# Kernel tuning notes

Hardware: AMD Instinct MI355X
Metric: run time of the kernel (lower is better)

Reference implementation:

```python
import jax, jax.numpy as jnp
import numpy as np

V, E, H, B, TE, TD = 32000, 256, 256, 32, 128, 64


def _gru_cell(x, h, Wi, Wh, bi, bh):
    # PyTorch GRU gate order: r, z, n
    gi = x @ Wi.T + bi            # [B, 3H]
    gh = h @ Wh.T + bh            # [B, 3H]
    i_r, i_z, i_n = jnp.split(gi, 3, axis=-1)
    h_r, h_z, h_n = jnp.split(gh, 3, axis=-1)
    r = jax.nn.sigmoid(i_r + h_r)
    z = jax.nn.sigmoid(i_z + h_z)
    n = jnp.tanh(i_n + r * h_n)
    return (1.0 - z) * n + z * h


def _run_gru(x_seq, h0, Wi, Wh, bi, bh, reverse=False):
    # x_seq: [B, T, D] -> outputs [B, T, H]
    xs = jnp.swapaxes(x_seq, 0, 1)  # [T, B, D]
    def step(h, x_t):
        h = _gru_cell(x_t, h, Wi, Wh, bi, bh)
        return h, h
    _, ys = jax.lax.scan(step, h0, xs, reverse=reverse)
    return jnp.swapaxes(ys, 0, 1)


def setup_inputs() -> dict:
    key = jax.random.key(0)
    ks = jax.random.split(key, 22)
    k = 1.0 / np.sqrt(H)
    u = lambda kk, shape, a: jax.random.uniform(kk, shape, jnp.float32, -a, a)
    return {
        'enc_in': jax.random.randint(ks[0], (B, TE), 0, V),
        'dec_in': jax.random.randint(ks[1], (B, TD), 0, V),
        'embed_W': u(ks[2], (V, E), 0.1),
        'Wi_f': u(ks[3], (3 * H, E), k), 'Wh_f': u(ks[4], (3 * H, H), k),
        'bi_f': u(ks[5], (3 * H,), k), 'bh_f': u(ks[6], (3 * H,), k),
        'Wi_b': u(ks[7], (3 * H, E), k), 'Wh_b': u(ks[8], (3 * H, H), k),
        'bi_b': u(ks[9], (3 * H,), k), 'bh_b': u(ks[10], (3 * H,), k),
        'Wi_d': u(ks[11], (3 * H, E + 2 * H), k), 'Wh_d': u(ks[12], (3 * H, H), k),
        'bi_d': u(ks[13], (3 * H,), k), 'bh_d': u(ks[14], (3 * H,), k),
        'W1_w': u(ks[15], (H, 2 * H), 1.0 / np.sqrt(2 * H)), 'W1_b': u(ks[16], (H,), 1.0 / np.sqrt(2 * H)),
        'W2_w': u(ks[17], (2 * H, H), k), 'W2_b': u(ks[18], (2 * H,), k),
        'lin_w': u(ks[19], (V, H), 0.1), 'lin_b': jnp.zeros((V,), jnp.float32),
    }


def reference(enc_in, dec_in, embed_W, Wi_f, Wh_f, bi_f, bh_f, Wi_b, Wh_b, bi_b, bh_b,
              Wi_d, Wh_d, bi_d, bh_d, W1_w, W1_b, W2_w, W2_b, lin_w, lin_b):
    # ---- encoder (bidirectional GRU, 1 layer) ----
    enc_emb = embed_W[enc_in]                                   # [B, TE, E]
    h0 = jnp.zeros((B, H), enc_emb.dtype)
    out_f = _run_gru(enc_emb, h0, Wi_f, Wh_f, bi_f, bh_f)       # [B, TE, H]
    out_b = _run_gru(enc_emb, h0, Wi_b, Wh_b, bi_b, bh_b, reverse=True)
    encoded = jnp.concatenate([out_f, out_b], axis=-1)          # [B, TE, 2H]

    # last valid state per example: encoded[i, sizes[i]-1]
    sizes = (enc_in > 0).sum(axis=1)                            # [B]
    last_states = encoded[jnp.arange(B), sizes - 1]             # [B, 2H]

    # ---- decoder with Luong attention (teacher forcing) ----
    dec_emb = embed_W[dec_in]                                   # [B, TD, E]
    h_init = last_states @ W1_w.T + W1_b                        # [B, H]
    ctx_init = jnp.zeros((B, 2 * H), enc_emb.dtype)

    def dec_step(carry, x_t):
        h, ctx = carry
        inp = jnp.concatenate([ctx, x_t], axis=-1)              # [B, E+2H]
        h = _gru_cell(inp, h, Wi_d, Wh_d, bi_d, bh_d)           # [B, H]
        comp = h @ W2_w.T + W2_b                                # [B, 2H]
        scores = jax.nn.softmax(jnp.einsum('bte,be->bt', encoded, comp), axis=-1)
        ctx = jnp.einsum('bt,bte->be', scores, encoded)          # [B, 2H]
        return (h, ctx), h

    _, outs = jax.lax.scan(dec_step, (h_init, ctx_init), jnp.swapaxes(dec_emb, 0, 1))
    outs = jnp.swapaxes(outs, 0, 1)                             # [B, TD, H]
    logits = outs @ lin_w.T + lin_b                             # [B, TD, V]
    return logits
```

## Files before the change

kernel.cpp:

```cpp
#include <hip/hip_runtime.h>
#include <hip/hip_bf16.h>

#define Vv 32000
#define Ee 256
#define Hh 256
#define Bb 32
#define TEe 128
#define TDd 64

typedef __attribute__((ext_vector_type(4))) float f32x4;
typedef __attribute__((ext_vector_type(8))) short short8;
typedef __attribute__((ext_vector_type(2))) unsigned int uint2v;
typedef __attribute__((ext_vector_type(4))) unsigned int uint4v;

static __device__ __forceinline__ unsigned short f2bf(float f){
  unsigned u = __float_as_uint(f);
  u += 0x7fffu + ((u >> 16) & 1u);
  return (unsigned short)(u >> 16);
}
static __device__ __forceinline__ unsigned pack2(float a, float b){
  return ((unsigned)f2bf(b) << 16) | (unsigned)f2bf(a);
}
static __device__ __forceinline__ float dot8(uint4v u, const float* hh){
  float s = 0.f;
  #pragma unroll
  for (int i = 0; i < 4; ++i){
    unsigned w = u[i];
    s = fmaf(__uint_as_float(w << 16),        hh[2*i],   s);
    s = fmaf(__uint_as_float(w & 0xffff0000u), hh[2*i+1], s);
  }
  return s;
}
static __device__ __forceinline__ float sigmoidf_(float x){
  return 1.f / (1.f + __expf(-x));
}

__global__ void k_sizes(const int* __restrict__ enc_in, int* __restrict__ sizes){
  int b = threadIdx.x;
  if (b < Bb){
    int c = 0;
    for (int t = 0; t < TEe; ++t) c += (enc_in[b*TEe + t] > 0);
    sizes[b] = c;
  }
}

__global__ void k_gather(const int* __restrict__ tok, const float* __restrict__ embW,
                         float* __restrict__ out, int rows){
  int i = blockIdx.x * 256 + threadIdx.x;
  int r = i >> 8, c = i & 255;
  if (r < rows) out[i] = embW[(size_t)tok[r]*Ee + c];
}

__global__ void k_extract_bf16(const float* __restrict__ src, unsigned short* __restrict__ dst,
                               int n){
  int i = blockIdx.x * 256 + threadIdx.x;
  if (i < n) dst[i] = f2bf(src[i]);
}

__global__ void k_chunkw(const float* __restrict__ src, unsigned short* __restrict__ dst, int rows){
  int idx = blockIdx.x * 256 + threadIdx.x;
  if (idx < rows * 256){
    int i = idx & 7, r = (idx >> 3) % rows, kb = idx / (rows * 8);
    dst[idx] = f2bf(src[(size_t)r*256 + kb*8 + i]);
  }
}

__global__ void k_projchunk(const float* __restrict__ in, unsigned short* __restrict__ out){
  int idx = blockIdx.x * 256 + threadIdx.x;
  int i = idx & 7;
  int t1 = idx >> 3;
  int n = t1 % 768;
  int t2 = t1 / 768;
  int kb = t2 & 15, b = t2 >> 4;
  out[idx] = f2bf(in[(size_t)(b*TEe + kb*8 + i)*768 + n]);
}

template<bool A_BF16, bool B_BF16, bool B_KMAJOR, bool OUT_BF16>
__global__ __launch_bounds__(256) void k_gemm(
  const void* __restrict__ Av, const void* __restrict__ Bv,
  const float* __restrict__ bias, void* __restrict__ Cv,
  int M, int N, int K, int lda, int ldb, int ldc)
{
  __shared__ unsigned short lA[128*40];
  __shared__ unsigned short lB[128*40];
  const int tid  = threadIdx.x;
  const int lane = tid & 63;
  const int w = tid >> 6, wr = w >> 1, wc = w & 1;
  const int m0 = blockIdx.y * 128, n0 = blockIdx.x * 128;
  f32x4 acc[4][4];
  #pragma unroll
  for (int i = 0; i < 4; ++i)
    #pragma unroll
    for (int j = 0; j < 4; ++j) acc[i][j] = (f32x4){0.f,0.f,0.f,0.f};

  for (int k0 = 0; k0 < K; k0 += 32){
    if (A_BF16){
      const unsigned short* A = (const unsigned short*)Av;
      #pragma unroll
      for (int it = 0; it < 2; ++it){
        int idx = tid + it*256; int r = idx >> 2, q = idx & 3;
        *(uint4v*)&lA[r*40 + q*8] = *(const uint4v*)(A + (size_t)(m0+r)*lda + k0 + q*8);
      }
    } else {
      const float* A = (const float*)Av;
      #pragma unroll
      for (int it = 0; it < 4; ++it){
        int idx = tid + it*256; int r = idx >> 3, q = idx & 7;
        f32x4 v = *(const f32x4*)(A + (size_t)(m0+r)*lda + k0 + q*4);
        uint2v pk; pk[0] = pack2(v[0], v[1]); pk[1] = pack2(v[2], v[3]);
        *(uint2v*)&lA[r*40 + q*4] = pk;
      }
    }
    if (B_KMAJOR){
      const float* Bp = (const float*)Bv;
      #pragma unroll
      for (int it = 0; it < 4; ++it){
        int idx = tid + it*256; int kk = idx >> 5, nq = idx & 31;
        f32x4 v = *(const f32x4*)(Bp + (size_t)(k0+kk)*ldb + n0 + nq*4);
        #pragma unroll
        for (int s2 = 0; s2 < 4; ++s2) lB[(nq*4+s2)*40 + kk] = f2bf(v[s2]);
      }
    } else if (B_BF16){
      const unsigned short* Bp = (const unsigned short*)Bv;
      #pragma unroll
      for (int it = 0; it < 2; ++it){
        int idx = tid + it*256; int r = idx >> 2, q = idx & 3;
        *(uint4v*)&lB[r*40 + q*8] = *(const uint4v*)(Bp + (size_t)(n0+r)*ldb + k0 + q*8);
      }
    } else {
      const float* Bp = (const float*)Bv;
      #pragma unroll
      for (int it = 0; it < 4; ++it){
        int idx = tid + it*256; int r = idx >> 3, q = idx & 7;
        f32x4 v = *(const f32x4*)(Bp + (size_t)(n0+r)*ldb + k0 + q*4);
        uint2v pk; pk[0] = pack2(v[0], v[1]); pk[1] = pack2(v[2], v[3]);
        *(uint2v*)&lB[r*40 + q*4] = pk;
      }
    }
    __syncthreads();
    short8 av[4], bv[4];
    #pragma unroll
    for (int i = 0; i < 4; ++i)
      av[i] = *(const short8*)&lA[(wr*64 + i*16 + (lane&15))*40 + (lane>>4)*8];
    #pragma unroll
    for (int j = 0; j < 4; ++j)
      bv[j] = *(const short8*)&lB[(wc*64 + j*16 + (lane&15))*40 + (lane>>4)*8];
    #pragma unroll
    for (int i = 0; i < 4; ++i)
      #pragma unroll
      for (int j = 0; j < 4; ++j)
        acc[i][j] = __builtin_amdgcn_mfma_f32_16x16x32_bf16(av[i], bv[j], acc[i][j], 0, 0, 0);
    __syncthreads();
  }
  #pragma unroll
  for (int i = 0; i < 4; ++i){
    #pragma unroll
    for (int j = 0; j < 4; ++j){
      int col = n0 + wc*64 + j*16 + (lane & 15);
      float bb = bias ? bias[col] : 0.f;
      #pragma unroll
      for (int r = 0; r < 4; ++r){
        int row = m0 + wr*64 + i*16 + (lane>>4)*4 + r;
        float v = acc[i][j][r] + bb;
        if (OUT_BF16) ((unsigned short*)Cv)[(size_t)row*ldc + col] = f2bf(v);
        else          ((float*)Cv)[(size_t)row*ldc + col] = v;
      }
    }
  }
}

__global__ __launch_bounds__(1024) void k_encoder(
  const unsigned short* __restrict__ Whf, const unsigned short* __restrict__ Whb,
  const float* __restrict__ bhf, const float* __restrict__ bhb,
  const float* __restrict__ gif, const float* __restrict__ gib,
  float* __restrict__ encoded)
{
  extern __shared__ char smem[];
  unsigned short* lw = (unsigned short*)smem;
  float* hA   = (float*)(smem + 131072);
  float* hB   = (float*)(smem + 132096);
  float* parA = (float*)(smem + 133120);
  float* parB = (float*)(smem + 137216);
  const int dir = blockIdx.x & 1, b = blockIdx.x >> 1;
  const unsigned short* Wh = dir ? Whb : Whf;
  const float* bh = dir ? bhb : bhf;
  const float* gi = dir ? gib : gif;
  const int T = threadIdx.x;
  const int rl = T & 255, q4 = T >> 8;
  const int rrh = T & 511, hf = T >> 9;
  const unsigned short* wsrc = Wh + (size_t)(hf*16)*6144 + (size_t)(256 + rrh)*8;
  uint4v wb[8];
  #pragma unroll
  for (int d = 0; d < 8; ++d) wb[d] = *(const uint4v*)(wsrc + (size_t)d*6144);
  for (int cc = T; cc < 256*32; cc += 1024){
    int r = cc >> 5, q = cc & 31;
    *(uint4v*)&lw[(r*32 + (q ^ (r & 31)))*8] = *(const uint4v*)(Wh + (size_t)q*6144 + r*8);
  }
  float bh0 = 0.f, bh1 = 0.f, bh2 = 0.f;
  if (T < 256){ bh0 = bh[T]; bh1 = bh[T+256]; bh2 = bh[T+512]; hA[T] = 0.f; }
  __syncthreads();
  const float* hc = hA; float* hn = hB;
  for (int s = 0; s < TEe; ++s){
    const int t = dir ? (TEe-1-s) : s;
    float aL = 0.f;
    #pragma unroll
    for (int i = 0; i < 8; ++i){
      const int ck = q4*8 + i;
      float hr[8];
      *(f32x4*)&hr[0] = *(const f32x4*)&hc[ck*8];
      *(f32x4*)&hr[4] = *(const f32x4*)&hc[ck*8+4];
      aL += dot8(*(const uint4v*)&lw[(rl*32 + (ck ^ (rl & 31)))*8], hr);
    }
    parA[q4*256 + rl] = aL;
    float aR = 0.f;
    const float* hh = hc + hf*128;
    #pragma unroll
    for (int q = 0; q < 16; ++q){
      float hr[8];
      *(f32x4*)&hr[0] = *(const f32x4*)&hh[q*8];
      *(f32x4*)&hr[4] = *(const f32x4*)&hh[q*8+4];
      aR += dot8(wb[q & 7], hr);
      wb[q & 7] = *(const uint4v*)(wsrc + (size_t)((q < 8) ? (q + 8) : (q - 8))*6144);
    }
    parB[hf*512 + rrh] = aR;
    __syncthreads();
    if (T < 256){
      const int j = T;
      const float* grow = gi + (size_t)(b*TEe + t)*768;
      const float A0 = parA[j] + parA[256+j] + parA[512+j] + parA[768+j] + bh0;
      const float A1 = parB[j] + parB[512+j] + bh1;
      const float A2 = parB[256+j] + parB[768+j] + bh2;
      const float r = sigmoidf_(grow[j] + A0);
      const float z = sigmoidf_(grow[j+256] + A1);
      const float n = tanhf(grow[j+512] + r*A2);
      const float hnew = (1.f - z)*n + z*hc[j];
      hn[j] = hnew;
      encoded[(size_t)(b*TEe + t)*512 + dir*256 + j] = hnew;
    }
    __syncthreads();
    const float* tmp = hc; hc = hn; hn = (float*)tmp;
  }
}

__global__ void k_encb2(const float* __restrict__ encoded, const float* __restrict__ W2b,
                        float* __restrict__ encb2){
  int r = blockIdx.x, l = threadIdx.x;
  const float* e = encoded + (size_t)r*512;
  float s = 0.f;
  for (int k = l; k < 512; k += 64) s += e[k]*W2b[k];
  for (int off = 32; off; off >>= 1) s += __shfl_down(s, off);
  if (l == 0) encb2[r] = s;
}

__global__ void k_hinit(const float* __restrict__ encoded, const int* __restrict__ sizes,
                        const float* __restrict__ W1w, const float* __restrict__ W1b,
                        float* __restrict__ h0){
  int b = blockIdx.x, o = threadIdx.x;
  int idx = sizes[b] - 1;
  idx = idx < 0 ? 0 : (idx > TEe-1 ? TEe-1 : idx);
  const float* ls = encoded + (size_t)(b*TEe + idx)*512;
  const float* wv = W1w + (size_t)o*512;
  float s = W1b[o];
  for (int k = 0; k < 512; k += 4){
    f32x4 a = *(const f32x4*)(ls + k);
    f32x4 w4 = *(const f32x4*)(wv + k);
    s = fmaf(a[0],w4[0], fmaf(a[1],w4[1], fmaf(a[2],w4[2], fmaf(a[3],w4[3], s))));
  }
  h0[b*256 + o] = s;
}

#define DNR 160
__global__ __launch_bounds__(1024) void k_decoder(
  const unsigned short* __restrict__ Whd, const float* __restrict__ bhd,
  const float* __restrict__ gidx,
  const unsigned short* __restrict__ encw2,
  const float* __restrict__ encb2,
  const unsigned short* __restrict__ projt,
  const float* __restrict__ h0,
  unsigned short* __restrict__ outs_bf)
{
  extern __shared__ char smem[];
  unsigned short* le = (unsigned short*)smem;
  unsigned short* lw = (unsigned short*)(smem + 65536);
  float* h   = (float*)(smem + 147456);
  float* par = (float*)(smem + 148480);
  float* gcs = (float*)(smem + 151552);
  float* p   = (float*)(smem + 154624);
  float* ebl = (float*)(smem + 155136);
  const int b = blockIdx.x, T = threadIdx.x;
  const unsigned short* ptc = projt + (size_t)b*98304;
  const unsigned short* wsrc = Whd + (size_t)T*8;
  const unsigned short* csrc = ptc + (size_t)T*8;
  uint4v wb[8], cb[4];
  const bool strm = (T >= DNR) && (T < 768);
  if (strm){
    #pragma unroll
    for (int d = 0; d < 8; ++d) wb[d] = *(const uint4v*)(wsrc + (size_t)d*6144);
  }
  if (T < 768){
    #pragma unroll
    for (int d = 0; d < 4; ++d) cb[d] = *(const uint4v*)(csrc + (size_t)d*6144);
  }
  for (int cc = T; cc < 128*32; cc += 1024){
    int r = cc >> 5, q = cc & 31;
    *(uint4v*)&le[(r*32 + (q ^ (r & 31)))*8] =
        *(const uint4v*)(encw2 + ((size_t)(b*TEe + r) << 8) + (q << 3));
  }
  for (int cc = T; cc < DNR*32; cc += 1024){
    int r = cc >> 5, q = cc & 31;
    *(uint4v*)&lw[(r*32 + (q ^ (r & 31)))*8] =
        *(const uint4v*)(Whd + (size_t)q*6144 + r*8);
  }
  for (int i = T; i < 256; i += 1024) h[i] = h0[b*256 + i];
  for (int i = T; i < 768; i += 1024) gcs[i] = 0.f;
  if (T < TEe) ebl[T] = encb2[b*TEe + T];
  float bh0 = 0.f, bh1 = 0.f, bh2 = 0.f;
  if (T < 256){ bh0 = bhd[T]; bh1 = bhd[T+256]; bh2 = bhd[T+512]; }
  __syncthreads();
  float g0 = 0.f, g1 = 0.f, g2 = 0.f;
  if (T < 256){
    const float* grow = gidx + (size_t)(b*TDd)*768;
    g0 = grow[T]; g1 = grow[T+256]; g2 = grow[T+512];
  }
  if (T < 768){
    float acc = 0.f;
    if (T < DNR){
      const unsigned short* lwr = lw + T*256;
      #pragma unroll
      for (int q = 0; q < 32; ++q){
        float hr[8];
        *(f32x4*)&hr[0] = *(const f32x4*)&h[q*8];
        *(f32x4*)&hr[4] = *(const f32x4*)&h[q*8+4];
        acc += dot8(*(const uint4v*)(lwr + ((q ^ (T & 31)) << 3)), hr);
      }
    } else {
      #pragma unroll
      for (int q = 0; q < 32; ++q){
        float hr[8];
        *(f32x4*)&hr[0] = *(const f32x4*)&h[q*8];
        *(f32x4*)&hr[4] = *(const f32x4*)&h[q*8+4];
        acc += dot8(wb[q & 7], hr);
        wb[q & 7] = *(const uint4v*)(wsrc + (size_t)((q < 24) ? (q + 8) : (q - 24))*6144);
      }
    }
    par[T] = acc;
  }
  __syncthreads();
  for (int t = 0; t < TDd; ++t){
    if (T < 256){
      const float A0 = par[T] + bh0;
      const float A1 = par[T+256] + bh1;
      const float A2 = par[T+512] + bh2;
      const float r = sigmoidf_(g0 + gcs[T] + A0);
      const float z = sigmoidf_(g1 + gcs[T+256] + A1);
      const float n = tanhf(g2 + gcs[T+512] + r*A2);
      const float hnew = (1.f - z)*n + z*h[T];
      h[T] = hnew;
      outs_bf[(size_t)(b*TDd + t)*256 + T] = f2bf(hnew);
    }
    if (t + 1 == TDd) break;
    __syncthreads();
    if (T < 768){
      if (T < 256){
        const float* grow = gidx + (size_t)(b*TDd + t + 1)*768;
        g0 = grow[T]; g1 = grow[T+256]; g2 = grow[T+512];
      }
      float acc = 0.f;
      if (T < DNR){
        const unsigned short* lwr = lw + T*256;
        #pragma unroll
        for (int q = 0; q < 32; ++q){
          float hr[8];
          *(f32x4*)&hr[0] = *(const f32x4*)&h[q*8];
          *(f32x4*)&hr[4] = *(const f32x4*)&h[q*8+4];
          acc += dot8(*(const uint4v*)(lwr + ((q ^ (T & 31)) << 3)), hr);
        }
      } else {
        #pragma unroll
        for (int q = 0; q < 32; ++q){
          float hr[8];
          *(f32x4*)&hr[0] = *(const f32x4*)&h[q*8];
          *(f32x4*)&hr[4] = *(const f32x4*)&h[q*8+4];
          acc += dot8(wb[q & 7], hr);
          wb[q & 7] = *(const uint4v*)(wsrc + (size_t)((q < 24) ? (q + 8) : (q - 24))*6144);
        }
      }
      par[T] = acc;
    } else {
      const int i = T - 768, pos = i >> 1, kh = i & 1;
      const unsigned short* er = le + pos*256;
      float s = 0.f;
      #pragma unroll
      for (int ii = 0; ii < 16; ++ii){
        const int q = kh*16 + ii;
        float hr[8];
        *(f32x4*)&hr[0] = *(const f32x4*)&h[q*8];
        *(f32x4*)&hr[4] = *(const f32x4*)&h[q*8+4];
        s += dot8(*(const uint4v*)(er + ((q ^ (pos & 31)) << 3)), hr);
      }
      s += __shfl_xor(s, 1);
      if (kh == 0) p[pos] = s + ebl[pos];
    }
    __syncthreads();
    if (T < 64){
      float m = fmaxf(p[T], p[T+64]);
      for (int off = 32; off; off >>= 1) m = fmaxf(m, __shfl_xor(m, off));
      float e0 = __expf(p[T] - m), e1 = __expf(p[T+64] - m);
      float ss = e0 + e1;
      for (int off = 32; off; off >>= 1) ss += __shfl_xor(ss, off);
      float inv = 1.f / ss;
      p[T] = e0*inv; p[T+64] = e1*inv;
    }
    __syncthreads();
    if (T < 768){
      float c = 0.f;
      #pragma unroll
      for (int q = 0; q < 16; ++q){
        float pr[8];
        *(f32x4*)&pr[0] = *(const f32x4*)&p[q*8];
        *(f32x4*)&pr[4] = *(const f32x4*)&p[q*8+4];
        c += dot8(cb[q & 3], pr);
        cb[q & 3] = *(const uint4v*)(csrc + (size_t)((q < 12) ? (q + 4) : (q - 12))*6144);
      }
      gcs[T] = c;
    }
    __syncthreads();
  }
}

extern "C" void kernel_launch(void* const* d_in, const int* in_sizes, int n_in,
                              void* d_out, int out_size, void* d_ws, size_t ws_size,
                              hipStream_t stream)
{
  (void)in_sizes; (void)n_in; (void)out_size;
  const int*   enc_in = (const int*)d_in[0];
  const int*   dec_in = (const int*)d_in[1];
  const float* embW   = (const float*)d_in[2];
  const float* Wi_f   = (const float*)d_in[3];
  const float* Wh_f   = (const float*)d_in[4];
  const float* bi_f   = (const float*)d_in[5];
  const float* bh_f   = (const float*)d_in[6];
  const float* Wi_b   = (const float*)d_in[7];
  const float* Wh_b   = (const float*)d_in[8];
  const float* bi_b   = (const float*)d_in[9];
  const float* bh_b   = (const float*)d_in[10];
  const float* Wi_d   = (const float*)d_in[11];
  const float* Wh_d   = (const float*)d_in[12];
  const float* bi_d   = (const float*)d_in[13];
  const float* bh_d   = (const float*)d_in[14];
  const float* W1_w   = (const float*)d_in[15];
  const float* W1_b   = (const float*)d_in[16];
  const float* W2_w   = (const float*)d_in[17];
  const float* W2_b   = (const float*)d_in[18];
  const float* lin_w  = (const float*)d_in[19];
  const float* lin_b  = (const float*)d_in[20];

  char* scr = (char*)d_out;
  float* emb_enc = (float*)(scr + 0);
  float* emb_dec = (float*)(scr + 4194304);
  float* gi_f    = (float*)(scr + 6291456);
  float* gi_b    = (float*)(scr + 18874368);
  float* gi_dx   = (float*)(scr + 31457280);
  float* enc     = (float*)(scr + 37748736);
  float* projf   = (float*)(scr + 46137344);
  unsigned short* whf_bf = (unsigned short*)(scr + 58720256);
  unsigned short* whb_bf = (unsigned short*)(scr + 59113472);
  unsigned short* whd_bf = (unsigned short*)(scr + 59506688);
  unsigned short* encw2  = (unsigned short*)(scr + 59899904);
  unsigned short* projt  = (unsigned short*)(scr + 61997056);
  float* encb2 = (float*)(scr + 68288512);
  int*   sizes = (int*)(scr + 68304896);
  float* h0    = (float*)(scr + 68305024);

  unsigned short* outs_bf = (unsigned short*)d_ws;
  unsigned short* lin_bf  = (unsigned short*)((char*)d_ws + (1<<20));
  const bool big = ws_size >= (size_t)(1<<20) + 16384000u + 1024u;

  hipFuncSetAttribute((const void*)k_encoder, hipFuncAttributeMaxDynamicSharedMemorySize, 141312);
  hipFuncSetAttribute((const void*)k_decoder, hipFuncAttributeMaxDynamicSharedMemorySize, 155648);

  k_sizes<<<1, 32, 0, stream>>>(enc_in, sizes);
  k_gather<<<Bb*TEe, 256, 0, stream>>>(enc_in, embW, emb_enc, Bb*TEe);
  k_gather<<<Bb*TDd, 256, 0, stream>>>(dec_in, embW, emb_dec, Bb*TDd);
  k_chunkw<<<768, 256, 0, stream>>>(Wh_f, whf_bf, 768);
  k_chunkw<<<768, 256, 0, stream>>>(Wh_b, whb_bf, 768);
  k_chunkw<<<768, 256, 0, stream>>>(Wh_d, whd_bf, 768);
  if (big) k_extract_bf16<<<32000, 256, 0, stream>>>(lin_w, lin_bf, 32000*256);

  k_gemm<false,false,false,false><<<dim3(6,32), 256, 0, stream>>>(
      emb_enc, Wi_f, bi_f, gi_f, 4096, 768, 256, 256, 256, 768);
  k_gemm<false,false,false,false><<<dim3(6,32), 256, 0, stream>>>(
      emb_enc, Wi_b, bi_b, gi_b, 4096, 768, 256, 256, 256, 768);
  k_gemm<false,false,false,false><<<dim3(6,16), 256, 0, stream>>>(
      emb_dec, Wi_d + 512, bi_d, gi_dx, 2048, 768, 256, 256, 768, 768);

  k_encoder<<<64, 1024, 141312, stream>>>(whf_bf, whb_bf, bh_f, bh_b, gi_f, gi_b, enc);
  k_encb2<<<Bb*TEe, 64, 0, stream>>>(enc, W2_b, encb2);

  k_gemm<false,false,true,true><<<dim3(2,32), 256, 0, stream>>>(
      enc, W2_w, nullptr, encw2, 4096, 256, 512, 512, 256, 256);
  k_gemm<false,false,false,false><<<dim3(6,32), 256, 0, stream>>>(
      enc, Wi_d, nullptr, projf, 4096, 768, 512, 512, 768, 768);
  k_projchunk<<<(Bb*16*768*8)/256, 256, 0, stream>>>(projf, projt);
  k_hinit<<<Bb, 256, 0, stream>>>(enc, sizes, W1_w, W1_b, h0);

  k_decoder<<<Bb, 1024, 155648, stream>>>(whd_bf, bh_d, gi_dx, encw2, encb2, projt, h0, outs_bf);

  if (big)
    k_gemm<true,true,false,false><<<dim3(250,16), 256, 0, stream>>>(
        outs_bf, lin_bf, lin_b, d_out, 2048, 32000, 256, 256, 256, 32000);
  else
    k_gemm<true,false,false,false><<<dim3(250,16), 256, 0, stream>>>(
        outs_bf, lin_w, lin_b, d_out, 2048, 32000, 256, 256, 256, 32000);
}
```

Measured before the change: 2.016 ms.

## Halve encoder and decoder block size to 512 threads with rebalanced row splits

The recurrent encoder and decoder kernels now launch 512 threads per block instead of 1024. Each thread takes on more of the recurrent matvec, with the work split differently across LDS-resident weight rows and register-streamed rows, and the partial-sum buffers and LDS layout change to match. The aim is cheaper per-step barriers and fewer partial reductions in the serial time loop. The cost is longer per-thread dot products and more register pressure, which may lengthen each step.

Result: no change. 1.994 ms (-1.1%).

```diff
diff --git a/kernel.cpp b/kernel.cpp
--- a/kernel.cpp
+++ b/kernel.cpp
@@ -169,7 +169,7 @@
   }
 }
 
-__global__ __launch_bounds__(1024) void k_encoder(
+__global__ __launch_bounds__(512, 1) void k_encoder(
   const unsigned short* __restrict__ Whf, const unsigned short* __restrict__ Whb,
   const float* __restrict__ bhf, const float* __restrict__ bhb,
   const float* __restrict__ gif, const float* __restrict__ gib,
@@ -179,20 +179,19 @@
   unsigned short* lw = (unsigned short*)smem;
   float* hA   = (float*)(smem + 131072);
   float* hB   = (float*)(smem + 132096);
-  float* parA = (float*)(smem + 133120);
-  float* parB = (float*)(smem + 137216);
+  float* parL = (float*)(smem + 133120);
+  float* parS = (float*)(smem + 135168);
   const int dir = blockIdx.x & 1, b = blockIdx.x >> 1;
   const unsigned short* Wh = dir ? Whb : Whf;
   const float* bh = dir ? bhb : bhf;
   const float* gi = dir ? gib : gif;
   const int T = threadIdx.x;
-  const int rl = T & 255, q4 = T >> 8;
-  const int rrh = T & 511, hf = T >> 9;
-  const unsigned short* wsrc = Wh + (size_t)(hf*16)*6144 + (size_t)(256 + rrh)*8;
+  const int rL = T >> 1, hfq = (T & 1)*16;
+  const unsigned short* wsrc = Wh + (size_t)(256 + T)*8;
   uint4v wb[8];
   #pragma unroll
   for (int d = 0; d < 8; ++d) wb[d] = *(const uint4v*)(wsrc + (size_t)d*6144);
-  for (int cc = T; cc < 256*32; cc += 1024){
+  for (int cc = T; cc < 256*32; cc += 512){
     int r = cc >> 5, q = cc & 31;
     *(uint4v*)&lw[(r*32 + (q ^ (r & 31)))*8] = *(const uint4v*)(Wh + (size_t)q*6144 + r*8);
   }
@@ -202,34 +201,38 @@
   const float* hc = hA; float* hn = hB;
   for (int s = 0; s < TEe; ++s){
     const int t = dir ? (TEe-1-s) : s;
-    float aL = 0.f;
-    #pragma unroll
-    for (int i = 0; i < 8; ++i){
-      const int ck = q4*8 + i;
-      float hr[8];
-      *(f32x4*)&hr[0] = *(const f32x4*)&hc[ck*8];
-      *(f32x4*)&hr[4] = *(const f32x4*)&hc[ck*8+4];
-      aL += dot8(*(const uint4v*)&lw[(rl*32 + (ck ^ (rl & 31)))*8], hr);
-    }
-    parA[q4*256 + rl] = aL;
-    float aR = 0.f;
-    const float* hh = hc + hf*128;
-    #pragma unroll
-    for (int q = 0; q < 16; ++q){
-      float hr[8];
-      *(f32x4*)&hr[0] = *(const f32x4*)&hh[q*8];
-      *(f32x4*)&hr[4] = *(const f32x4*)&hh[q*8+4];
-      aR += dot8(wb[q & 7], hr);
-      wb[q & 7] = *(const uint4v*)(wsrc + (size_t)((q < 8) ? (q + 8) : (q - 8))*6144);
-    }
-    parB[hf*512 + rrh] = aR;
+    {
+      const unsigned short* lwr = lw + rL*256;
+      float a = 0.f;
+      #pragma unroll
+      for (int i = 0; i < 16; ++i){
+        const int q = hfq + i;
+        float hr[8];
+        *(f32x4*)&hr[0] = *(const f32x4*)&hc[q*8];
+        *(f32x4*)&hr[4] = *(const f32x4*)&hc[q*8+4];
+        a += dot8(*(const uint4v*)(lwr + ((q ^ (rL & 31)) << 3)), hr);
+      }
+      parL[(T & 1)*256 + rL] = a;
+    }
+    {
+      float a = 0.f;
+      #pragma unroll
+      for (int q = 0; q < 32; ++q){
+        float hr[8];
+        *(f32x4*)&hr[0] = *(const f32x4*)&hc[q*8];
+        *(f32x4*)&hr[4] = *(const f32x4*)&hc[q*8+4];
+        a += dot8(wb[q & 7], hr);
+        wb[q & 7] = *(const uint4v*)(wsrc + (size_t)((q < 24) ? (q + 8) : (q - 24))*6144);
+      }
+      parS[T] = a;
+    }
     __syncthreads();
     if (T < 256){
       const int j = T;
       const float* grow = gi + (size_t)(b*TEe + t)*768;
-      const float A0 = parA[j] + parA[256+j] + parA[512+j] + parA[768+j] + bh0;
-      const float A1 = parB[j] + parB[512+j] + bh1;
-      const float A2 = parB[256+j] + parB[768+j] + bh2;
+      const float A0 = parL[j] + parL[256+j] + bh0;
+      const float A1 = parS[j] + bh1;
+      const float A2 = parS[256+j] + bh2;
       const float r = sigmoidf_(grow[j] + A0);
       const float z = sigmoidf_(grow[j+256] + A1);
       const float n = tanhf(grow[j+512] + r*A2);
@@ -269,8 +272,8 @@
   h0[b*256 + o] = s;
 }
 
-#define DNR 160
-__global__ __launch_bounds__(1024) void k_decoder(
+#define DLR 128
+__global__ __launch_bounds__(512, 1) void k_decoder(
   const unsigned short* __restrict__ Whd, const float* __restrict__ bhd,
   const float* __restrict__ gidx,
   const unsigned short* __restrict__ encw2,
@@ -282,37 +285,43 @@
   extern __shared__ char smem[];
   unsigned short* le = (unsigned short*)smem;
   unsigned short* lw = (unsigned short*)(smem + 65536);
-  float* h   = (float*)(smem + 147456);
-  float* par = (float*)(smem + 148480);
-  float* gcs = (float*)(smem + 151552);
-  float* p   = (float*)(smem + 154624);
-  float* ebl = (float*)(smem + 155136);
+  float* h    = (float*)(smem + 131072);
+  float* parL = (float*)(smem + 132096);
+  float* parS1= (float*)(smem + 134144);
+  float* parS2= (float*)(smem + 136192);
+  float* gcs  = (float*)(smem + 138240);
+  float* cpar = (float*)(smem + 140288);
+  float* p    = (float*)(smem + 142336);
+  float* ebl  = (float*)(smem + 142848);
   const int b = blockIdx.x, T = threadIdx.x;
   const unsigned short* ptc = projt + (size_t)b*98304;
-  const unsigned short* wsrc = Whd + (size_t)T*8;
-  const unsigned short* csrc = ptc + (size_t)T*8;
-  uint4v wb[8], cb[4];
-  const bool strm = (T >= DNR) && (T < 768);
-  if (strm){
-    #pragma unroll
-    for (int d = 0; d < 8; ++d) wb[d] = *(const uint4v*)(wsrc + (size_t)d*6144);
-  }
-  if (T < 768){
-    #pragma unroll
-    for (int d = 0; d < 4; ++d) cb[d] = *(const uint4v*)(csrc + (size_t)d*6144);
-  }
-  for (int cc = T; cc < 128*32; cc += 1024){
+  const unsigned short* wsrcM = Whd + (size_t)(DLR + T)*8;
+  const int trow = 640 + (T >> 2), tq = (T & 3)*8;
+  const unsigned short* wsrcT = Whd + (size_t)trow*8;
+  const unsigned short* csrcM = ptc + (size_t)T*8;
+  const int crow = 512 + (T >> 1), cq = (T & 1)*8;
+  const unsigned short* csrcT = ptc + (size_t)crow*8;
+  uint4v wb[8], wb2[2], cb[4], cb2[2];
+  #pragma unroll
+  for (int d = 0; d < 8; ++d) wb[d] = *(const uint4v*)(wsrcM + (size_t)d*6144);
+  wb2[0] = *(const uint4v*)(wsrcT + (size_t)tq*6144);
+  wb2[1] = *(const uint4v*)(wsrcT + (size_t)(tq+1)*6144);
+  #pragma unroll
+  for (int d = 0; d < 4; ++d) cb[d] = *(const uint4v*)(csrcM + (size_t)d*6144);
+  cb2[0] = *(const uint4v*)(csrcT + (size_t)cq*6144);
+  cb2[1] = *(const uint4v*)(csrcT + (size_t)(cq+1)*6144);
+  for (int cc = T; cc < 128*32; cc += 512){
     int r = cc >> 5, q = cc & 31;
     *(uint4v*)&le[(r*32 + (q ^ (r & 31)))*8] =
         *(const uint4v*)(encw2 + ((size_t)(b*TEe + r) << 8) + (q << 3));
   }
-  for (int cc = T; cc < DNR*32; cc += 1024){
+  for (int cc = T; cc < DLR*32; cc += 512){
     int r = cc >> 5, q = cc & 31;
     *(uint4v*)&lw[(r*32 + (q ^ (r & 31)))*8] =
         *(const uint4v*)(Whd + (size_t)q*6144 + r*8);
   }
-  for (int i = T; i < 256; i += 1024) h[i] = h0[b*256 + i];
-  for (int i = T; i < 768; i += 1024) gcs[i] = 0.f;
+  for (int i = T; i < 256; i += 512) h[i] = h0[b*256 + i];
+  gcs[T] = 0.f; cpar[T] = 0.f;
   if (T < TEe) ebl[T] = encb2[b*TEe + T];
   float bh0 = 0.f, bh1 = 0.f, bh2 = 0.f;
   if (T < 256){ bh0 = bhd[T]; bh1 = bhd[T+256]; bh2 = bhd[T+512]; }
@@ -322,84 +331,91 @@
     const float* grow = gidx + (size_t)(b*TDd)*768;
     g0 = grow[T]; g1 = grow[T+256]; g2 = grow[T+512];
   }
-  if (T < 768){
-    float acc = 0.f;
-    if (T < DNR){
-      const unsigned short* lwr = lw + T*256;
-      #pragma unroll
-      for (int q = 0; q < 32; ++q){
-        float hr[8];
-        *(f32x4*)&hr[0] = *(const f32x4*)&h[q*8];
-        *(f32x4*)&hr[4] = *(const f32x4*)&h[q*8+4];
-        acc += dot8(*(const uint4v*)(lwr + ((q ^ (T & 31)) << 3)), hr);
-      }
-    } else {
-      #pragma unroll
-      for (int q = 0; q < 32; ++q){
-        float hr[8];
-        *(f32x4*)&hr[0] = *(const f32x4*)&h[q*8];
-        *(f32x4*)&hr[4] = *(const f32x4*)&h[q*8+4];
-        acc += dot8(wb[q & 7], hr);
-        wb[q & 7] = *(const uint4v*)(wsrc + (size_t)((q < 24) ? (q + 8) : (q - 24))*6144);
-      }
-    }
-    par[T] = acc;
-  }
+  #define DOTS_BODY                                                            \
+  {                                                                            \
+    { const int rL2 = T >> 2, qb = (T & 3)*8;                                  \
+      const unsigned short* lwr = lw + rL2*256;                                \
+      float a = 0.f;                                                           \
+      _Pragma("unroll")                                                        \
+      for (int i = 0; i < 8; ++i){                                             \
+        const int q = qb + i;                                                  \
+        float hr[8];                                                           \
+        *(f32x4*)&hr[0] = *(const f32x4*)&h[q*8];                              \
+        *(f32x4*)&hr[4] = *(const f32x4*)&h[q*8+4];                            \
+        a += dot8(*(const uint4v*)(lwr + ((q ^ (rL2 & 31)) << 3)), hr);        \
+      }                                                                        \
+      parL[(T & 3)*128 + rL2] = a;                                             \
+    }                                                                          \
+    { float a = 0.f;                                                           \
+      _Pragma("unroll")                                                        \
+      for (int q = 0; q < 32; ++q){                                            \
+        float hr[8];                                                           \
+        *(f32x4*)&hr[0] = *(const f32x4*)&h[q*8];                              \
+        *(f32x4*)&hr[4] = *(const f32x4*)&h[q*8+4];                            \
+        a += dot8(wb[q & 7], hr);                                              \
+        wb[q & 7] = *(const uint4v*)(wsrcM + (size_t)((q < 24) ? (q + 8) : (q - 24))*6144); \
+      }                                                                        \
+      parS1[T] = a;                                                            \
+    }                                                                          \
+    { float a = 0.f;                                                           \
+      _Pragma("unroll")                                                        \
+      for (int i = 0; i < 8; ++i){                                             \
+        const int q = tq + i;                                                  \
+        float hr[8];                                                           \
+        *(f32x4*)&hr[0] = *(const f32x4*)&h[q*8];                              \
+        *(f32x4*)&hr[4] = *(const f32x4*)&h[q*8+4];                            \
+        a += dot8(wb2[i & 1], hr);                                             \
+        wb2[i & 1] = *(const uint4v*)(wsrcT + (size_t)(tq + ((i < 6) ? (i + 2) : (i - 6)))*6144); \
+      }                                                                        \
+      parS2[(T & 3)*128 + (T >> 2)] = a;                                       \
+    }                                                                          \
+  }
+  DOTS_BODY
   __syncthreads();
   for (int t = 0; t < TDd; ++t){
     if (T < 256){
-      const float A0 = par[T] + bh0;
-      const float A1 = par[T+256] + bh1;
-      const float A2 = par[T+512] + bh2;
-      const float r = sigmoidf_(g0 + gcs[T] + A0);
-      const float z = sigmoidf_(g1 + gcs[T+256] + A1);
-      const float n = tanhf(g2 + gcs[T+512] + r*A2);
-      const float hnew = (1.f - z)*n + z*h[T];
-      h[T] = hnew;
-      outs_bf[(size_t)(b*TDd + t)*256 + T] = f2bf(hnew);
+      const int j = T;
+      float A0, A2;
+      if (j < 128){
+        A0 = parL[j] + parL[128+j] + parL[256+j] + parL[384+j];
+        A2 = parS1[384+j];
+      } else {
+        A0 = parS1[j-128];
+        A2 = parS2[j-128] + parS2[j] + parS2[j+128] + parS2[j+256];
+      }
+      const float A1 = parS1[128+j];
+      const float gcr = gcs[j];
+      const float gcz = gcs[256+j];
+      const float gcn = cpar[j] + cpar[256+j];
+      const float r = sigmoidf_(g0 + gcr + A0 + bh0);
+      const float z = sigmoidf_(g1 + gcz + A1 + bh1);
+      const float n = tanhf(g2 + gcn + r*(A2 + bh2));
+      const float hnew = (1.f - z)*n + z*h[j];
+      h[j] = hnew;
+      outs_bf[(size_t)(b*TDd + t)*256 + j] = f2bf(hnew);
     }
     if (t + 1 == TDd) break;
     __syncthreads();
-    if (T < 768){
-      if (T < 256){
-        const float* grow = gidx + (size_t)(b*TDd + t + 1)*768;
-        g0 = grow[T]; g1 = grow[T+256]; g2 = grow[T+512];
-      }
-      float acc = 0.f;
-      if (T < DNR){
-        const unsigned short* lwr = lw + T*256;
-        #pragma unroll
-        for (int q = 0; q < 32; ++q){
-          float hr[8];
-          *(f32x4*)&hr[0] = *(const f32x4*)&h[q*8];
-          *(f32x4*)&hr[4] = *(const f32x4*)&h[q*8+4];
-          acc += dot8(*(const uint4v*)(lwr + ((q ^ (T & 31)) << 3)), hr);
-        }
-      } else {
-        #pragma unroll
-        for (int q = 0; q < 32; ++q){
-          float hr[8];
-          *(f32x4*)&hr[0] = *(const f32x4*)&h[q*8];
-          *(f32x4*)&hr[4] = *(const f32x4*)&h[q*8+4];
-          acc += dot8(wb[q & 7], hr);
-          wb[q & 7] = *(const uint4v*)(wsrc + (size_t)((q < 24) ? (q + 8) : (q - 24))*6144);
-        }
-      }
-      par[T] = acc;
-    } else {
-      const int i = T - 768, pos = i >> 1, kh = i & 1;
+    if (T < 256){
+      const float* grow = gidx + (size_t)(b*TDd + t + 1)*768;
+      g0 = grow[T]; g1 = grow[T+256]; g2 = grow[T+512];
+    }
+    DOTS_BODY
+    {
+      const int pos = T >> 2, kq = (T & 3)*8;
       const unsigned short* er = le + pos*256;
       float s = 0.f;
       #pragma unroll
-      for (int ii = 0; ii < 16; ++ii){
-        const int q = kh*16 + ii;
+      for (int i = 0; i < 8; ++i){
+        const int q = kq + i;
         float hr[8];
         *(f32x4*)&hr[0] = *(const f32x4*)&h[q*8];
         *(f32x4*)&hr[4] = *(const f32x4*)&h[q*8+4];
         s += dot8(*(const uint4v*)(er + ((q ^ (pos & 31)) << 3)), hr);
       }
       s += __shfl_xor(s, 1);
-      if (kh == 0) p[pos] = s + ebl[pos];
+      s += __shfl_xor(s, 2);
+      if ((T & 3) == 0) p[pos] = s + ebl[pos];
     }
     __syncthreads();
     if (T < 64){
@@ -412,7 +428,7 @@
       p[T] = e0*inv; p[T+64] = e1*inv;
     }
     __syncthreads();
-    if (T < 768){
+    {
       float c = 0.f;
       #pragma unroll
       for (int q = 0; q < 16; ++q){
@@ -420,12 +436,24 @@
         *(f32x4*)&pr[0] = *(const f32x4*)&p[q*8];
         *(f32x4*)&pr[4] = *(const f32x4*)&p[q*8+4];
         c += dot8(cb[q & 3], pr);
-        cb[q & 3] = *(const uint4v*)(csrc + (size_t)((q < 12) ? (q + 4) : (q - 12))*6144);
+        cb[q & 3] = *(const uint4v*)(csrcM + (size_t)((q < 12) ? (q + 4) : (q - 12))*6144);
       }
       gcs[T] = c;
-    }
-    __syncthreads();
-  }
+      float c2 = 0.f;
+      #pragma unroll
+      for (int i = 0; i < 8; ++i){
+        const int q = cq + i;
+        float pr[8];
+        *(f32x4*)&pr[0] = *(const f32x4*)&p[q*8];
+        *(f32x4*)&pr[4] = *(const f32x4*)&p[q*8+4];
+        c2 += dot8(cb2[i & 1], pr);
+        cb2[i & 1] = *(const uint4v*)(csrcT + (size_t)(cq + ((i < 6) ? (i + 2) : (i - 6)))*6144);
+      }
+      cpar[(T & 1)*256 + (T >> 1)] = c2;
+    }
+    __syncthreads();
+  }
+  #undef DOTS_BODY
 }
 
 extern "C" void kernel_launch(void* const* d_in, const int* in_sizes, int n_in,
@@ -476,8 +504,8 @@
   unsigned short* lin_bf  = (unsigned short*)((char*)d_ws + (1<<20));
   const bool big = ws_size >= (size_t)(1<<20) + 16384000u + 1024u;
 
-  hipFuncSetAttribute((const void*)k_encoder, hipFuncAttributeMaxDynamicSharedMemorySize, 141312);
-  hipFuncSetAttribute((const void*)k_decoder, hipFuncAttributeMaxDynamicSharedMemorySize, 155648);
+  hipFuncSetAttribute((const void*)k_encoder, hipFuncAttributeMaxDynamicSharedMemorySize, 137216);
+  hipFuncSetAttribute((const void*)k_decoder, hipFuncAttributeMaxDynamicSharedMemorySize, 143360);
 
   k_sizes<<<1, 32, 0, stream>>>(enc_in, sizes);
   k_gather<<<Bb*TEe, 256, 0, stream>>>(enc_in, embW, emb_enc, Bb*TEe);
@@ -494,7 +522,7 @@
   k_gemm<false,false,false,false><<<dim3(6,16), 256, 0, stream>>>(
       emb_dec, Wi_d + 512, bi_d, gi_dx, 2048, 768, 256, 256, 768, 768);
 
-  k_encoder<<<64, 1024, 141312, stream>>>(whf_bf, whb_bf, bh_f, bh_b, gi_f, gi_b, enc);
+  k_encoder<<<64, 512, 137216, stream>>>(whf_bf, whb_bf, bh_f, bh_b, gi_f, gi_b, enc);
   k_encb2<<<Bb*TEe, 64, 0, stream>>>(enc, W2_b, encb2);
 
   k_gemm<false,false,true,true><<<dim3(2,32), 256, 0, stream>>>(
@@ -504,7 +532,7 @@
   k_projchunk<<<(Bb*16*768*8)/256, 256, 0, stream>>>(projf, projt);
   k_hinit<<<Bb, 256, 0, stream>>>(enc, sizes, W1_w, W1_b, h0);
 
-  k_decoder<<<Bb, 1024, 155648, stream>>>(whd_bf, bh_d, gi_dx, encw2, encb2, projt, h0, outs_bf);
+  k_decoder<<<Bb, 512, 143360, stream>>>(whd_bf, bh_d, gi_dx, encw2, encb2, projt, h0, outs_bf);
 
   if (big)
     k_gemm<true,true,false,false><<<dim3(250,16), 256, 0, stream>>>(
```
